# Optimization experiments

Hardware: AMD Instinct MI355X
Metric: run time of the kernel (lower is better)

The kernel has to match this reference:

```python
import jax, jax.numpy as jnp
import numpy as np

N = 100000   # nodes
E = 1600000  # edges (before self-loops)
C = 128      # num_node_features == graph_hidden_channels (residuals require equality)
NHID = 512
NOUT = 256
B = 512      # number of graphs in the batch
BN_EPS = 1e-5


def setup_inputs() -> dict:
    key = jax.random.key(0)
    ks = list(jax.random.split(key, 32))
    k = iter(ks)

    def w(shape, fan_in):
        return jax.random.normal(next(k), shape, jnp.float32) * (1.0 / np.sqrt(fan_in))

    inp = {}
    inp["x"] = jax.random.normal(next(k), (N, C), jnp.float32)
    inp["edge_index"] = jax.random.randint(next(k), (2, E), 0, N, jnp.int32)
    inp["batch"] = jnp.sort(jax.random.randint(next(k), (N,), 0, B, jnp.int32))
    # three GCN layers: lin weight [C,C], bias [C], BN gamma/beta
    for i in (1, 2, 3):
        inp[f"W{i}"] = w((C, C), C)
        inp[f"b{i}"] = jnp.zeros((C,), jnp.float32)
        inp[f"g{i}"] = jnp.ones((C,), jnp.float32)
        inp[f"be{i}"] = jnp.zeros((C,), jnp.float32)
    # GAT (1 head)
    inp["Wa"] = w((C, C), C)
    inp["asrc"] = w((C,), C)
    inp["adst"] = w((C,), C)
    inp["ba"] = jnp.zeros((C,), jnp.float32)
    inp["ga"] = jnp.ones((C,), jnp.float32)
    inp["bea"] = jnp.zeros((C,), jnp.float32)
    # MLP head
    inp["Wh1"] = w((C, NHID), C)
    inp["bh1"] = jnp.zeros((NHID,), jnp.float32)
    inp["Wm0"] = w((NHID, NHID), NHID)
    inp["bm0"] = jnp.zeros((NHID,), jnp.float32)
    inp["Wm1"] = w((NHID, NHID), NHID)
    inp["bm1"] = jnp.zeros((NHID,), jnp.float32)
    inp["Wo"] = w((NHID, NOUT), NHID)
    inp["bo"] = jnp.zeros((NOUT,), jnp.float32)
    return inp


def _add_self_loops(edge_index):
    loops = jnp.arange(N, dtype=edge_index.dtype)
    src = jnp.concatenate([edge_index[0], loops])
    dst = jnp.concatenate([edge_index[1], loops])
    return src, dst


def _gcn(x, src, dst, W, b):
    # PyG GCNConv: add self-loops, D^-1/2 (A+I) D^-1/2 (x W) + b
    deg = jax.ops.segment_sum(jnp.ones_like(dst, jnp.float32), dst, num_segments=N)
    dinv = jax.lax.rsqrt(jnp.maximum(deg, 1.0))
    norm = dinv[src] * dinv[dst]                      # [E+N]
    h = x @ W                                         # [N,C]
    msg = h[src] * norm[:, None]                      # gather + scale
    return jax.ops.segment_sum(msg, dst, num_segments=N) + b


def _gat(x, src, dst, W, asrc, adst, b):
    # PyG GATConv, heads=1: self-loops, alpha = softmax_dst(leaky_relu(a_s.h_j + a_d.h_i))
    h = x @ W                                         # [N,C]
    es = (h * asrc).sum(-1)                           # [N]
    ed = (h * adst).sum(-1)
    e = jax.nn.leaky_relu(es[src] + ed[dst], 0.2)     # [E+N]
    m = jax.ops.segment_max(e, dst, num_segments=N)
    ex = jnp.exp(e - m[dst])
    s = jax.ops.segment_sum(ex, dst, num_segments=N)
    alpha = ex / (s[dst] + 1e-16)
    out = jax.ops.segment_sum(h[src] * alpha[:, None], dst, num_segments=N)
    return out + b


def _bn(h, g, be):
    # BatchNorm in training mode: biased batch stats over node dim
    m = h.mean(0)
    v = ((h - m) ** 2).mean(0)
    return (h - m) * jax.lax.rsqrt(v + BN_EPS) * g + be


def reference(x, edge_index, batch,
              W1, b1, g1, be1, W2, b2, g2, be2, W3, b3, g3, be3,
              Wa, asrc, adst, ba, ga, bea,
              Wh1, bh1, Wm0, bm0, Wm1, bm1, Wo, bo):
    src, dst = _add_self_loops(edge_index)
    x = jax.nn.relu(_bn(_gcn(x, src, dst, W1, b1), g1, be1)) + x
    x = jax.nn.relu(_bn(_gcn(x, src, dst, W2, b2), g2, be2)) + x
    x = jax.nn.relu(_bn(_gcn(x, src, dst, W3, b3), g3, be3)) + x
    x = jax.nn.relu(_bn(_gat(x, src, dst, Wa, asrc, adst, ba), ga, bea)) + x
    # global mean pool over graphs
    sums = jax.ops.segment_sum(x, batch, num_segments=B)
    cnt = jax.ops.segment_sum(jnp.ones((N,), jnp.float32), batch, num_segments=B)
    x = sums / jnp.maximum(cnt, 1.0)[:, None]         # [B,C]
    x = jax.nn.relu(x @ Wh1 + bh1)
    x = jax.nn.relu(x @ Wm0 + bm0)
    x = jax.nn.relu(x @ Wm1 + bm1)
    return x @ Wo + bo                                # [B,NOUT]
```

## Files before the change

kernel.cpp:

```cpp
#include <hip/hip_runtime.h>

#define N_NODES 100000
#define N_EDGES 1600000
#define CCH     128
#define BG      512
#define NHID    512
#define NOUT    256
#define BN_EPS  1e-5f

typedef __attribute__((ext_vector_type(8))) short s16x8;
typedef __attribute__((ext_vector_type(4))) float f32x4;

static __device__ __forceinline__ float leaky(float x) { return x > 0.f ? x : 0.2f * x; }
static __device__ __forceinline__ uint32_t bfr16(float x) {
  uint32_t u = __float_as_uint(x);
  u += 0x7fffu + ((u >> 16) & 1u);
  return u >> 16;
}
static __device__ __forceinline__ uint32_t pack2(float a, float b) {
  return bfr16(a) | (bfr16(b) << 16);
}
static __device__ __forceinline__ float blo(uint32_t u) { return __uint_as_float(u << 16); }
static __device__ __forceinline__ float bhi(uint32_t u) { return __uint_as_float(u & 0xffff0000u); }

__global__ void hist_kernel(const int* __restrict__ dst, int* __restrict__ indeg) {
  int e = blockIdx.x * 256 + threadIdx.x;
  if (e < N_EDGES) atomicAdd(&indeg[dst[e]], 1);
}

__global__ __launch_bounds__(256) void scan_chunks(const int* __restrict__ indeg,
                                                   int* __restrict__ rowstart,
                                                   int* __restrict__ chunksum) {
  int tid = threadIdx.x;
  int base = blockIdx.x * 1024 + tid * 4;
  int4 v;
  if (base + 3 < N_NODES) {
    v = *(const int4*)(indeg + base);
  } else {
    v.x = (base + 0 < N_NODES) ? indeg[base + 0] : 0;
    v.y = (base + 1 < N_NODES) ? indeg[base + 1] : 0;
    v.z = (base + 2 < N_NODES) ? indeg[base + 2] : 0;
    v.w = (base + 3 < N_NODES) ? indeg[base + 3] : 0;
  }
  int s = v.x + v.y + v.z + v.w;
  __shared__ int ss[256];
  ss[tid] = s;
  __syncthreads();
  for (int off = 1; off < 256; off <<= 1) {
    int t = (tid >= off) ? ss[tid - off] : 0;
    __syncthreads();
    ss[tid] += t;
    __syncthreads();
  }
  int excl = ss[tid] - s;
  if (base + 0 < N_NODES) rowstart[base + 0] = excl;
  if (base + 1 < N_NODES) rowstart[base + 1] = excl + v.x;
  if (base + 2 < N_NODES) rowstart[base + 2] = excl + v.x + v.y;
  if (base + 3 < N_NODES) rowstart[base + 3] = excl + v.x + v.y + v.z;
  if (tid == 255) chunksum[blockIdx.x] = ss[255];
}

__global__ void scan_sums(int* __restrict__ chunksum, int nch) {
  __shared__ int ss[128];
  int tid = threadIdx.x;
  int v = (tid < nch) ? chunksum[tid] : 0;
  ss[tid] = v;
  __syncthreads();
  for (int off = 1; off < 128; off <<= 1) {
    int t = (tid >= off) ? ss[tid - off] : 0;
    __syncthreads();
    ss[tid] += t;
    __syncthreads();
  }
  if (tid < nch) chunksum[tid] = ss[tid] - v;
}

__global__ void scan_add(int* __restrict__ rowstart, const int* __restrict__ chunksum) {
  int i = blockIdx.x * 256 + threadIdx.x;
  if (i < N_NODES)      rowstart[i] += chunksum[i >> 10];
  else if (i == N_NODES) rowstart[N_NODES] = N_EDGES;
}

__global__ void compute_dinv(const int* __restrict__ indeg, float* __restrict__ dinv) {
  int i = blockIdx.x * 256 + threadIdx.x;
  if (i < N_NODES) dinv[i] = rsqrtf((float)(indeg[i] + 1));
}

__global__ void scatter_edges(const int* __restrict__ src, const int* __restrict__ dst,
                              const int* __restrict__ rowstart, int* __restrict__ cursor,
                              const float* __restrict__ dinv, int2* __restrict__ csr_sw) {
  int e = blockIdx.x * 256 + threadIdx.x;
  if (e < N_EDGES) {
    int d = dst[e];
    int s = src[e];
    int p = rowstart[d] + atomicAdd(&cursor[d], 1);
    float w = dinv[s] * dinv[d];
    csr_sw[p] = make_int2(s, __float_as_int(w));
  }
}

__global__ void cast_bf16_kernel(const float2* __restrict__ x2, uint32_t* __restrict__ xb) {
  size_t idx = (size_t)blockIdx.x * 256 + threadIdx.x;
  if (idx >= (size_t)N_NODES * 64) return;
  float2 v = x2[idx];
  xb[idx] = pack2(v.x, v.y);
}

__global__ void pack_w_kernel(const float* __restrict__ W, unsigned short* __restrict__ Wp) {
  int t = blockIdx.x * 256 + threadIdx.x;
  if (t >= 2048) return;
  int lane = t & 63;
  int ks = (t >> 6) & 3;
  int nt = t >> 8;
  int c = nt * 16 + (lane & 15);
  int kb = ks * 32 + (lane >> 4) * 8;
#pragma unroll
  for (int i = 0; i < 8; ++i)
    Wp[(size_t)t * 8 + i] = (unsigned short)bfr16(W[(size_t)(kb + i) * 128 + c]);
}

__global__ __launch_bounds__(256) void gemm_mfma(const uint32_t* __restrict__ Ab,
                                                 const unsigned short* __restrict__ Wp,
                                                 uint32_t* __restrict__ Hb,
                                                 int M) {
  int wave = threadIdx.x >> 6, lane = threadIdx.x & 63;
  int row0 = blockIdx.x * 128 + wave * 32;
  const unsigned short* A16 = (const unsigned short*)Ab;

  f32x4 acc[2][8];
#pragma unroll
  for (int mt = 0; mt < 2; ++mt)
#pragma unroll
    for (int nt = 0; nt < 8; ++nt) acc[mt][nt] = (f32x4){0.f, 0.f, 0.f, 0.f};

  s16x8 a[2][4];
  int r = lane & 15, ko = (lane >> 4) * 8;
#pragma unroll
  for (int mt = 0; mt < 2; ++mt) {
    int row = row0 + mt * 16 + r;
    bool v = row < M;
    const unsigned short* ap = A16 + (size_t)row * 128 + ko;
#pragma unroll
    for (int ks = 0; ks < 4; ++ks) {
      s16x8 af = {0, 0, 0, 0, 0, 0, 0, 0};
      if (v) af = *(const s16x8*)(ap + ks * 32);
      a[mt][ks] = af;
    }
  }
#pragma unroll
  for (int ks = 0; ks < 4; ++ks) {
#pragma unroll
    for (int nt = 0; nt < 8; ++nt) {
      s16x8 b = *(const s16x8*)(Wp + ((size_t)(nt * 4 + ks) * 64 + lane) * 8);
      acc[0][nt] = __builtin_amdgcn_mfma_f32_16x16x32_bf16(a[0][ks], b, acc[0][nt], 0, 0, 0);
      acc[1][nt] = __builtin_amdgcn_mfma_f32_16x16x32_bf16(a[1][ks], b, acc[1][nt], 0, 0, 0);
    }
  }
#pragma unroll
  for (int mt = 0; mt < 2; ++mt) {
#pragma unroll
    for (int nt = 0; nt < 8; ++nt) {
#pragma unroll
      for (int reg = 0; reg < 4; ++reg) {
        float v0 = acc[mt][nt][reg];
        float v1 = __shfl_xor(v0, 1);
        int row = row0 + mt * 16 + (lane >> 4) * 4 + reg;
        int col = nt * 16 + (lane & 15);
        if (!(lane & 1) && row < M)
          Hb[(size_t)row * 64 + (col >> 1)] = pack2(v0, v1);
      }
    }
  }
}

__global__ __launch_bounds__(256) void gcn_agg(const uint2* __restrict__ Hb2,
                                               const int* __restrict__ rowstart,
                                               const int2* __restrict__ csr_sw,
                                               const float* __restrict__ dinv,
                                               float4* __restrict__ agg4,
                                               float* __restrict__ stats) {
  int tid = threadIdx.x;
  int lane = tid & 63;
  int hl = lane & 31;
  int half = lane >> 5;
  int gw = (blockIdx.x * 256 + tid) >> 6;
  int nw = (gridDim.x * 256) >> 6;
  float s0 = 0, s1 = 0, s2 = 0, s3 = 0, q0 = 0, q1 = 0, q2 = 0, q3 = 0;
  for (int pi = gw; pi < N_NODES / 2; pi += nw) {
    int n = 2 * pi + half;
    int e0 = rowstart[n], e1 = rowstart[n + 1];
    int len = e1 - e0;
    int G = (len + 3) >> 2;
    int Gmax = max(G, __shfl_xor(G, 32));
    int ecl = (len > 0) ? (e1 - 1) : 0;
    float di = dinv[n];
    uint2 hs = Hb2[(size_t)n * 32 + hl];
    float ws = di * di;
    float c0 = blo(hs.x) * ws, c1 = bhi(hs.x) * ws;
    float c2 = blo(hs.y) * ws, c3 = bhi(hs.y) * ws;
    int sI0, sI1, sI2, sI3;
    float w0, w1, w2, w3;
    {
      int e = e0;
      int2 pa = csr_sw[e < e1 ? e : ecl];
      int2 pb = csr_sw[e + 1 < e1 ? e + 1 : ecl];
      int2 pc = csr_sw[e + 2 < e1 ? e + 2 : ecl];
      int2 pd = csr_sw[e + 3 < e1 ? e + 3 : ecl];
      sI0 = pa.x; w0 = (e < e1) ? __int_as_float(pa.y) : 0.f;
      sI1 = pb.x; w1 = (e + 1 < e1) ? __int_as_float(pb.y) : 0.f;
      sI2 = pc.x; w2 = (e + 2 < e1) ? __int_as_float(pc.y) : 0.f;
      sI3 = pd.x; w3 = (e + 3 < e1) ? __int_as_float(pd.y) : 0.f;
    }
    for (int g = 0; g < Gmax; ++g) {
      uint2 r0 = Hb2[(size_t)sI0 * 32 + hl];
      uint2 r1 = Hb2[(size_t)sI1 * 32 + hl];
      uint2 r2 = Hb2[(size_t)sI2 * 32 + hl];
      uint2 r3 = Hb2[(size_t)sI3 * 32 + hl];
      float cw0 = w0, cw1 = w1, cw2 = w2, cw3 = w3;
      int e = e0 + (g + 1) * 4;
      int2 pa = csr_sw[e < e1 ? e : ecl];
      int2 pb = csr_sw[e + 1 < e1 ? e + 1 : ecl];
      int2 pc = csr_sw[e + 2 < e1 ? e + 2 : ecl];
      int2 pd = csr_sw[e + 3 < e1 ? e + 3 : ecl];
      sI0 = pa.x; w0 = (e < e1) ? __int_as_float(pa.y) : 0.f;
      sI1 = pb.x; w1 = (e + 1 < e1) ? __int_as_float(pb.y) : 0.f;
      sI2 = pc.x; w2 = (e + 2 < e1) ? __int_as_float(pc.y) : 0.f;
      sI3 = pd.x; w3 = (e + 3 < e1) ? __int_as_float(pd.y) : 0.f;
      c0 = fmaf(blo(r0.x), cw0, c0); c1 = fmaf(bhi(r0.x), cw0, c1);
      c2 = fmaf(blo(r0.y), cw0, c2); c3 = fmaf(bhi(r0.y), cw0, c3);
      c0 = fmaf(blo(r1.x), cw1, c0); c1 = fmaf(bhi(r1.x), cw1, c1);
      c2 = fmaf(blo(r1.y), cw1, c2); c3 = fmaf(bhi(r1.y), cw1, c3);
      c0 = fmaf(blo(r2.x), cw2, c0); c1 = fmaf(bhi(r2.x), cw2, c1);
      c2 = fmaf(blo(r2.y), cw2, c2); c3 = fmaf(bhi(r2.y), cw2, c3);
      c0 = fmaf(blo(r3.x), cw3, c0); c1 = fmaf(bhi(r3.x), cw3, c1);
      c2 = fmaf(blo(r3.y), cw3, c2); c3 = fmaf(bhi(r3.y), cw3, c3);
    }
    agg4[(size_t)n * 32 + hl] = make_float4(c0, c1, c2, c3);
    s0 += c0; s1 += c1; s2 += c2; s3 += c3;
    q0 += c0 * c0; q1 += c1 * c1; q2 += c2 * c2; q3 += c3 * c3;
  }
  s0 += __shfl_xor(s0, 32); s1 += __shfl_xor(s1, 32);
  s2 += __shfl_xor(s2, 32); s3 += __shfl_xor(s3, 32);
  q0 += __shfl_xor(q0, 32); q1 += __shfl_xor(q1, 32);
  q2 += __shfl_xor(q2, 32); q3 += __shfl_xor(q3, 32);
  __shared__ float red[4][128];
  int w = tid >> 6;
  if (half == 0) {
    red[w][4 * hl + 0] = s0; red[w][4 * hl + 1] = s1;
    red[w][4 * hl + 2] = s2; red[w][4 * hl + 3] = s3;
  }
  __syncthreads();
  if (w == 0) {
    float a = red[0][2 * lane] + red[1][2 * lane] + red[2][2 * lane] + red[3][2 * lane];
    float b = red[0][2 * lane + 1] + red[1][2 * lane + 1] + red[2][2 * lane + 1] + red[3][2 * lane + 1];
    atomicAdd(&stats[2 * lane], a);
    atomicAdd(&stats[2 * lane + 1], b);
  }
  __syncthreads();
  if (half == 0) {
    red[w][4 * hl + 0] = q0; red[w][4 * hl + 1] = q1;
    red[w][4 * hl + 2] = q2; red[w][4 * hl + 3] = q3;
  }
  __syncthreads();
  if (w == 0) {
    float a = red[0][2 * lane] + red[1][2 * lane] + red[2][2 * lane] + red[3][2 * lane];
    float b = red[0][2 * lane + 1] + red[1][2 * lane + 1] + red[2][2 * lane + 1] + red[3][2 * lane + 1];
    atomicAdd(&stats[128 + 2 * lane], a);
    atomicAdd(&stats[128 + 2 * lane + 1], b);
  }
}

__global__ __launch_bounds__(256) void compute_esed(const uint32_t* __restrict__ Hb,
                                                    const float* __restrict__ asrc,
                                                    const float* __restrict__ adst,
                                                    float* __restrict__ es, float* __restrict__ ed) {
  int lane = threadIdx.x & 63;
  int gwave = (blockIdx.x * 256 + threadIdx.x) >> 6;
  if (gwave >= N_NODES) return;
  float2 av = ((const float2*)asrc)[lane];
  float2 dv = ((const float2*)adst)[lane];
  uint32_t hv = Hb[(size_t)gwave * 64 + lane];
  float hx = blo(hv), hy = bhi(hv);
  float e_s = hx * av.x + hy * av.y;
  float e_d = hx * dv.x + hy * dv.y;
  for (int off = 32; off; off >>= 1) {
    e_s += __shfl_down(e_s, off);
    e_d += __shfl_down(e_d, off);
  }
  if (lane == 0) { es[gwave] = e_s; ed[gwave] = e_d; }
}

__global__ void gat_pack_kernel(int2* __restrict__ sw, const float* __restrict__ es) {
  int e = blockIdx.x * 256 + threadIdx.x;
  if (e < N_EDGES) {
    int2 v = sw[e];
    v.y = __float_as_int(es[v.x]);
    sw[e] = v;
  }
}

__global__ __launch_bounds__(256) void gat_agg(const uint2* __restrict__ Hb2,
                                               const int* __restrict__ rowstart,
                                               const int2* __restrict__ gpack,
                                               const float* __restrict__ es,
                                               const float* __restrict__ ed,
                                               float4* __restrict__ agg4,
                                               float* __restrict__ stats) {
  int tid = threadIdx.x;
  int lane = tid & 63;
  int hl = lane & 31;
  int half = lane >> 5;
  int gw = (blockIdx.x * 256 + tid) >> 6;
  int nw = (gridDim.x * 256) >> 6;
  float s0 = 0, s1 = 0, s2 = 0, s3 = 0, q0 = 0, q1 = 0, q2 = 0, q3 = 0;
  for (int pi = gw; pi < N_NODES / 2; pi += nw) {
    int n = 2 * pi + half;
    int e0 = rowstart[n], e1 = rowstart[n + 1];
    int len = e1 - e0;
    int G = (len + 3) >> 2;
    int Gmax = max(G, __shfl_xor(G, 32));
    int ecl = (len > 0) ? (e1 - 1) : 0;
    float edi = ed[n], esi = es[n];
    float wself = __expf(leaky(esi + edi));
    float wsum = (hl == 0) ? wself : 0.f;
    for (int e = e0 + hl; e < e1; e += 32)
      wsum += __expf(leaky(__int_as_float(gpack[e].y) + edi));
#pragma unroll
    for (int off = 16; off; off >>= 1) wsum += __shfl_xor(wsum, off);
    float inv = 1.f / (wsum + 1e-16f);

    uint2 hs = Hb2[(size_t)n * 32 + hl];
    float wS = wself * inv;
    float c0 = blo(hs.x) * wS, c1 = bhi(hs.x) * wS;
    float c2 = blo(hs.y) * wS, c3 = bhi(hs.y) * wS;
    int sI0, sI1, sI2, sI3;
    float w0, w1, w2, w3;
    {
      int e = e0;
      int2 pa = gpack[e < e1 ? e : ecl];
      int2 pb = gpack[e + 1 < e1 ? e + 1 : ecl];
      int2 pc = gpack[e + 2 < e1 ? e + 2 : ecl];
      int2 pd = gpack[e + 3 < e1 ? e + 3 : ecl];
      sI0 = pa.x; w0 = (e < e1) ? __expf(leaky(__int_as_float(pa.y) + edi)) * inv : 0.f;
      sI1 = pb.x; w1 = (e + 1 < e1) ? __expf(leaky(__int_as_float(pb.y) + edi)) * inv : 0.f;
      sI2 = pc.x; w2 = (e + 2 < e1) ? __expf(leaky(__int_as_float(pc.y) + edi)) * inv : 0.f;
      sI3 = pd.x; w3 = (e + 3 < e1) ? __expf(leaky(__int_as_float(pd.y) + edi)) * inv : 0.f;
    }
    for (int g = 0; g < Gmax; ++g) {
      uint2 r0 = Hb2[(size_t)sI0 * 32 + hl];
      uint2 r1 = Hb2[(size_t)sI1 * 32 + hl];
      uint2 r2 = Hb2[(size_t)sI2 * 32 + hl];
      uint2 r3 = Hb2[(size_t)sI3 * 32 + hl];
      float cw0 = w0, cw1 = w1, cw2 = w2, cw3 = w3;
      int e = e0 + (g + 1) * 4;
      int2 pa = gpack[e < e1 ? e : ecl];
      int2 pb = gpack[e + 1 < e1 ? e + 1 : ecl];
      int2 pc = gpack[e + 2 < e1 ? e + 2 : ecl];
      int2 pd = gpack[e + 3 < e1 ? e + 3 : ecl];
      sI0 = pa.x; w0 = (e < e1) ? __expf(leaky(__int_as_float(pa.y) + edi)) * inv : 0.f;
      sI1 = pb.x; w1 = (e + 1 < e1) ? __expf(leaky(__int_as_float(pb.y) + edi)) * inv : 0.f;
      sI2 = pc.x; w2 = (e + 2 < e1) ? __expf(leaky(__int_as_float(pc.y) + edi)) * inv : 0.f;
      sI3 = pd.x; w3 = (e + 3 < e1) ? __expf(leaky(__int_as_float(pd.y) + edi)) * inv : 0.f;
      c0 = fmaf(blo(r0.x), cw0, c0); c1 = fmaf(bhi(r0.x), cw0, c1);
      c2 = fmaf(blo(r0.y), cw0, c2); c3 = fmaf(bhi(r0.y), cw0, c3);
      c0 = fmaf(blo(r1.x), cw1, c0); c1 = fmaf(bhi(r1.x), cw1, c1);
      c2 = fmaf(blo(r1.y), cw1, c2); c3 = fmaf(bhi(r1.y), cw1, c3);
      c0 = fmaf(blo(r2.x), cw2, c0); c1 = fmaf(bhi(r2.x), cw2, c1);
      c2 = fmaf(blo(r2.y), cw2, c2); c3 = fmaf(bhi(r2.y), cw2, c3);
      c0 = fmaf(blo(r3.x), cw3, c0); c1 = fmaf(bhi(r3.x), cw3, c1);
      c2 = fmaf(blo(r3.y), cw3, c2); c3 = fmaf(bhi(r3.y), cw3, c3);
    }
    agg4[(size_t)n * 32 + hl] = make_float4(c0, c1, c2, c3);
    s0 += c0; s1 += c1; s2 += c2; s3 += c3;
    q0 += c0 * c0; q1 += c1 * c1; q2 += c2 * c2; q3 += c3 * c3;
  }
  s0 += __shfl_xor(s0, 32); s1 += __shfl_xor(s1, 32);
  s2 += __shfl_xor(s2, 32); s3 += __shfl_xor(s3, 32);
  q0 += __shfl_xor(q0, 32); q1 += __shfl_xor(q1, 32);
  q2 += __shfl_xor(q2, 32); q3 += __shfl_xor(q3, 32);
  __shared__ float red[4][128];
  int w = tid >> 6;
  if (half == 0) {
    red[w][4 * hl + 0] = s0; red[w][4 * hl + 1] = s1;
    red[w][4 * hl + 2] = s2; red[w][4 * hl + 3] = s3;
  }
  __syncthreads();
  if (w == 0) {
    float a = red[0][2 * lane] + red[1][2 * lane] + red[2][2 * lane] + red[3][2 * lane];
    float b = red[0][2 * lane + 1] + red[1][2 * lane + 1] + red[2][2 * lane + 1] + red[3][2 * lane + 1];
    atomicAdd(&stats[2 * lane], a);
    atomicAdd(&stats[2 * lane + 1], b);
  }
  __syncthreads();
  if (half == 0) {
    red[w][4 * hl + 0] = q0; red[w][4 * hl + 1] = q1;
    red[w][4 * hl + 2] = q2; red[w][4 * hl + 3] = q3;
  }
  __syncthreads();
  if (w == 0) {
    float a = red[0][2 * lane] + red[1][2 * lane] + red[2][2 * lane] + red[3][2 * lane];
    float b = red[0][2 * lane + 1] + red[1][2 * lane + 1] + red[2][2 * lane + 1] + red[3][2 * lane + 1];
    atomicAdd(&stats[128 + 2 * lane], a);
    atomicAdd(&stats[128 + 2 * lane + 1], b);
  }
}

__global__ void bn_relu_res(const float4* __restrict__ agg4, const float* __restrict__ stats,
                            const float* __restrict__ gamma, const float* __restrict__ beta,
                            uint2* __restrict__ xb) {
  size_t idx = (size_t)blockIdx.x * 256 + threadIdx.x;
  if (idx >= (size_t)N_NODES * 32) return;
  int c = ((int)(idx & 31)) * 4;
  const float n_inv = 1.f / (float)N_NODES;
  float sc[4], bc[4];
#pragma unroll
  for (int k = 0; k < 4; ++k) {
    float m = stats[c + k] * n_inv;
    float v = stats[128 + c + k] * n_inv - m * m;
    sc[k] = gamma[c + k] * rsqrtf(v + BN_EPS);
    bc[k] = beta[c + k] - m * sc[k];
  }
  float4 a = agg4[idx];
  uint2 xi = xb[idx];
  float r0 = fmaxf(fmaf(a.x, sc[0], bc[0]), 0.f) + blo(xi.x);
  float r1 = fmaxf(fmaf(a.y, sc[1], bc[1]), 0.f) + bhi(xi.x);
  float r2 = fmaxf(fmaf(a.z, sc[2], bc[2]), 0.f) + blo(xi.y);
  float r3 = fmaxf(fmaf(a.w, sc[3], bc[3]), 0.f) + bhi(xi.y);
  xb[idx] = make_uint2(pack2(r0, r1), pack2(r2, r3));
}

__global__ void graph_starts(const int* __restrict__ batch, int* __restrict__ gstart) {
  int n = blockIdx.x * 256 + threadIdx.x;
  if (n >= N_NODES) return;
  int b = batch[n];
  int bp = (n == 0) ? -1 : batch[n - 1];
  for (int g = bp + 1; g <= b; ++g) gstart[g] = n;
  if (n == N_NODES - 1) {
    for (int g = b + 1; g <= BG; ++g) gstart[g] = N_NODES;
  }
}

__global__ __launch_bounds__(256) void pool_kernel(const uint32_t* __restrict__ xb,
                                                   const int* __restrict__ gstart,
                                                   float* __restrict__ pooled) {
  int g = blockIdx.x;
  int c = threadIdx.x & 127;
  int half = threadIdx.x >> 7;
  int s = gstart[g], e = gstart[g + 1];
  float acc = 0.f;
  for (int n = s + half; n < e; n += 2) {
    uint32_t u = xb[(size_t)n * 64 + (c >> 1)];
    acc += (c & 1) ? bhi(u) : blo(u);
  }
  __shared__ float red[256];
  red[threadIdx.x] = acc;
  __syncthreads();
  if (half == 0) {
    float v = red[c] + red[128 + c];
    int cnt = e - s;
    pooled[(size_t)g * 128 + c] = v / fmaxf((float)cnt, 1.f);
  }
}

template <int RELU, int BIAS>
__global__ __launch_bounds__(256) void gemm_f32(const float* __restrict__ A,
                                                const float* __restrict__ W,
                                                const float* __restrict__ bias,
                                                float* __restrict__ Cmat,
                                                int M, int K, int N) {
  __shared__ float As[32][128];
  __shared__ float Bs[32][128];
  int tid = threadIdx.x;
  int row0 = blockIdx.x * 128, col0 = blockIdx.y * 128;
  int tx = tid & 15, ty = tid >> 4;
  float acc[8][8];
#pragma unroll
  for (int i = 0; i < 8; ++i)
#pragma unroll
    for (int j = 0; j < 8; ++j) acc[i][j] = 0.f;

  for (int k0 = 0; k0 < K; k0 += 32) {
    {
      int r = tid >> 1;
      int kseg = (tid & 1) * 16;
      bool valid = (row0 + r) < M;
      const float* ap = A + (size_t)(row0 + r) * K + k0 + kseg;
#pragma unroll
      for (int q = 0; q < 4; ++q) {
        float4 v;
        if (valid) v = *(const float4*)(ap + q * 4);
        else { v.x = v.y = v.z = v.w = 0.f; }
        As[kseg + q * 4 + 0][r] = v.x;
        As[kseg + q * 4 + 1][r] = v.y;
        As[kseg + q * 4 + 2][r] = v.z;
        As[kseg + q * 4 + 3][r] = v.w;
      }
    }
    {
      int kk = tid >> 3;
      int seg = (tid & 7) * 16;
      const float* wp = W + (size_t)(k0 + kk) * N + col0 + seg;
#pragma unroll
      for (int q = 0; q < 4; ++q)
        *(float4*)&Bs[kk][seg + q * 4] = *(const float4*)(wp + q * 4);
    }
    __syncthreads();
#pragma unroll
    for (int kk = 0; kk < 32; ++kk) {
      float4 a0 = *(const float4*)&As[kk][ty * 4];
      float4 a1 = *(const float4*)&As[kk][64 + ty * 4];
      float4 b0 = *(const float4*)&Bs[kk][tx * 4];
      float4 b1 = *(const float4*)&Bs[kk][64 + tx * 4];
      float av[8] = {a0.x, a0.y, a0.z, a0.w, a1.x, a1.y, a1.z, a1.w};
      float bv[8] = {b0.x, b0.y, b0.z, b0.w, b1.x, b1.y, b1.z, b1.w};
#pragma unroll
      for (int i = 0; i < 8; ++i)
#pragma unroll
        for (int j = 0; j < 8; ++j) acc[i][j] = fmaf(av[i], bv[j], acc[i][j]);
    }
    __syncthreads();
  }
#pragma unroll
  for (int i = 0; i < 8; ++i) {
    int r = row0 + ((i < 4) ? (ty * 4 + i) : (64 + ty * 4 + i - 4));
    if (r >= M) continue;
#pragma unroll
    for (int j = 0; j < 8; ++j) {
      int c = col0 + ((j < 4) ? (tx * 4 + j) : (64 + tx * 4 + j - 4));
      float v = acc[i][j];
      if (BIAS) v += bias[c];
      if (RELU) v = fmaxf(v, 0.f);
      Cmat[(size_t)r * N + c] = v;
    }
  }
}

extern "C" void kernel_launch(void* const* d_in, const int* in_sizes, int n_in,
                              void* d_out, int out_size, void* d_ws, size_t ws_size,
                              hipStream_t stream) {
  const float* x_in  = (const float*)d_in[0];
  const int*   eidx  = (const int*)d_in[1];
  const int*   batch = (const int*)d_in[2];
  const float* W1 = (const float*)d_in[3];
  const float* g1 = (const float*)d_in[5];
  const float* be1 = (const float*)d_in[6];
  const float* W2 = (const float*)d_in[7];
  const float* g2 = (const float*)d_in[9];
  const float* be2 = (const float*)d_in[10];
  const float* W3 = (const float*)d_in[11];
  const float* g3 = (const float*)d_in[13];
  const float* be3 = (const float*)d_in[14];
  const float* Wa = (const float*)d_in[15];
  const float* asrc = (const float*)d_in[16];
  const float* adst = (const float*)d_in[17];
  const float* ga = (const float*)d_in[19];
  const float* bea = (const float*)d_in[20];
  const float* Wh1 = (const float*)d_in[21];
  const float* bh1 = (const float*)d_in[22];
  const float* Wm0 = (const float*)d_in[23];
  const float* bm0 = (const float*)d_in[24];
  const float* Wm1 = (const float*)d_in[25];
  const float* bm1 = (const float*)d_in[26];
  const float* Wo = (const float*)d_in[27];
  const float* bo = (const float*)d_in[28];

  const int* src = eidx;
  const int* dst = eidx + N_EDGES;

  char* p = (char*)d_ws;
  auto alloc = [&](size_t bytes) {
    char* r = p;
    p += (bytes + 255) & ~(size_t)255;
    return r;
  };
  uint32_t* Hb     = (uint32_t*)alloc((size_t)N_NODES * 64 * 4);
  uint32_t* xb     = (uint32_t*)alloc((size_t)N_NODES * 64 * 4);
  float* agg       = (float*)alloc((size_t)N_NODES * CCH * 4);
  int2*  csr_sw    = (int2*)alloc((size_t)N_EDGES * 8);
  int*   rowstart  = (int*)alloc((size_t)(N_NODES + 1) * 4);
  int*   indeg     = (int*)alloc((size_t)2 * N_NODES * 4);
  int*   cursor    = indeg + N_NODES;
  float* dinv      = (float*)alloc((size_t)N_NODES * 4);
  float* es        = (float*)alloc((size_t)N_NODES * 4);
  float* ed        = (float*)alloc((size_t)N_NODES * 4);
  int*   chunksum  = (int*)alloc(128 * 4);
  float* stats     = (float*)alloc(4 * 256 * 4);
  int*   gstart    = (int*)alloc((BG + 1) * 4);
  float* pooled    = (float*)alloc((size_t)BG * CCH * 4);
  float* m1        = (float*)alloc((size_t)BG * NHID * 4);
  float* m2        = (float*)alloc((size_t)BG * NHID * 4);
  unsigned short* Wp1 = (unsigned short*)alloc(2048 * 8 * 2);
  unsigned short* Wp2 = (unsigned short*)alloc(2048 * 8 * 2);
  unsigned short* Wp3 = (unsigned short*)alloc(2048 * 8 * 2);
  unsigned short* Wp4 = (unsigned short*)alloc(2048 * 8 * 2);

  hipMemsetAsync(indeg, 0, (size_t)2 * N_NODES * 4, stream);
  hipMemsetAsync(stats, 0, 4 * 256 * 4, stream);

  hist_kernel<<<(N_EDGES + 255) / 256, 256, 0, stream>>>(dst, indeg);
  scan_chunks<<<98, 256, 0, stream>>>(indeg, rowstart, chunksum);
  scan_sums<<<1, 128, 0, stream>>>(chunksum, 98);
  scan_add<<<(N_NODES + 256) / 256, 256, 0, stream>>>(rowstart, chunksum);
  compute_dinv<<<(N_NODES + 255) / 256, 256, 0, stream>>>(indeg, dinv);
  scatter_edges<<<(N_EDGES + 255) / 256, 256, 0, stream>>>(src, dst, rowstart, cursor, dinv, csr_sw);

  const int el2_blocks = (N_NODES * 64 + 255) / 256;
  const int el4_blocks = (N_NODES * 32 + 255) / 256;
  cast_bf16_kernel<<<el2_blocks, 256, 0, stream>>>((const float2*)x_in, xb);
  pack_w_kernel<<<8, 256, 0, stream>>>(W1, Wp1);
  pack_w_kernel<<<8, 256, 0, stream>>>(W2, Wp2);
  pack_w_kernel<<<8, 256, 0, stream>>>(W3, Wp3);
  pack_w_kernel<<<8, 256, 0, stream>>>(Wa, Wp4);

  const int gemm_blocks_m = (N_NODES + 127) / 128;
  const int AGG_BLOCKS = 2048;

  const unsigned short* Wps[3] = {Wp1, Wp2, Wp3};
  const float* gs[3] = {g1, g2, g3};
  const float* bes[3] = {be1, be2, be3};
  for (int l = 0; l < 3; ++l) {
    gemm_mfma<<<gemm_blocks_m, 256, 0, stream>>>(xb, Wps[l], Hb, N_NODES);
    gcn_agg<<<AGG_BLOCKS, 256, 0, stream>>>((const uint2*)Hb, rowstart, csr_sw, dinv,
                                            (float4*)agg, stats + l * 256);
    bn_relu_res<<<el4_blocks, 256, 0, stream>>>((const float4*)agg, stats + l * 256,
                                                gs[l], bes[l], (uint2*)xb);
  }

  gemm_mfma<<<gemm_blocks_m, 256, 0, stream>>>(xb, Wp4, Hb, N_NODES);
  compute_esed<<<(N_NODES + 3) / 4, 256, 0, stream>>>(Hb, asrc, adst, es, ed);
  gat_pack_kernel<<<(N_EDGES + 255) / 256, 256, 0, stream>>>(csr_sw, es);
  gat_agg<<<AGG_BLOCKS, 256, 0, stream>>>((const uint2*)Hb, rowstart, csr_sw, es, ed,
                                          (float4*)agg, stats + 3 * 256);
  bn_relu_res<<<el4_blocks, 256, 0, stream>>>((const float4*)agg, stats + 3 * 256,
                                              ga, bea, (uint2*)xb);

  graph_starts<<<(N_NODES + 255) / 256, 256, 0, stream>>>(batch, gstart);
  pool_kernel<<<BG, 256, 0, stream>>>(xb, gstart, pooled);

  gemm_f32<1, 1><<<dim3(4, 4), 256, 0, stream>>>(pooled, Wh1, bh1, m1, BG, CCH, NHID);
  gemm_f32<1, 1><<<dim3(4, 4), 256, 0, stream>>>(m1, Wm0, bm0, m2, BG, NHID, NHID);
  gemm_f32<1, 1><<<dim3(4, 4), 256, 0, stream>>>(m2, Wm1, bm1, m1, BG, NHID, NHID);
  gemm_f32<0, 1><<<dim3(4, 2), 256, 0, stream>>>(m1, Wo, bo, (float*)d_out, BG, NHID, NOUT);
}
```

Before: 1.182 ms.

## Deepen gather prefetch in aggregation and precompute GAT edge weights per node

```diff
diff --git a/kernel.cpp b/kernel.cpp
--- a/kernel.cpp
+++ b/kernel.cpp
@@ -173,12 +173,15 @@
   }
 }
 
-__global__ __launch_bounds__(256) void gcn_agg(const uint2* __restrict__ Hb2,
-                                               const int* __restrict__ rowstart,
-                                               const int2* __restrict__ csr_sw,
-                                               const float* __restrict__ dinv,
-                                               float4* __restrict__ agg4,
-                                               float* __restrict__ stats) {
+template <int GAT>
+__global__ __launch_bounds__(256) void agg_kernel(const uint2* __restrict__ Hb2,
+                                                  const int* __restrict__ rowstart,
+                                                  const int2* __restrict__ pack,
+                                                  const float* __restrict__ dinv,
+                                                  const float* __restrict__ wselfa,
+                                                  const float* __restrict__ winv,
+                                                  float4* __restrict__ agg4,
+                                                  float* __restrict__ stats) {
   int tid = threadIdx.x;
   int lane = tid & 63;
   int hl = lane & 31;
@@ -193,48 +196,81 @@
     int G = (len + 3) >> 2;
     int Gmax = max(G, __shfl_xor(G, 32));
     int ecl = (len > 0) ? (e1 - 1) : 0;
-    float di = dinv[n];
+    float selfw, fscale;
+    if (GAT) { selfw = wselfa[n]; fscale = winv[n]; }
+    else     { float di = dinv[n]; selfw = di * di; fscale = 1.f; }
     uint2 hs = Hb2[(size_t)n * 32 + hl];
-    float ws = di * di;
-    float c0 = blo(hs.x) * ws, c1 = bhi(hs.x) * ws;
-    float c2 = blo(hs.y) * ws, c3 = bhi(hs.y) * ws;
-    int sI0, sI1, sI2, sI3;
-    float w0, w1, w2, w3;
-    {
-      int e = e0;
-      int2 pa = csr_sw[e < e1 ? e : ecl];
-      int2 pb = csr_sw[e + 1 < e1 ? e + 1 : ecl];
-      int2 pc = csr_sw[e + 2 < e1 ? e + 2 : ecl];
-      int2 pd = csr_sw[e + 3 < e1 ? e + 3 : ecl];
-      sI0 = pa.x; w0 = (e < e1) ? __int_as_float(pa.y) : 0.f;
-      sI1 = pb.x; w1 = (e + 1 < e1) ? __int_as_float(pb.y) : 0.f;
-      sI2 = pc.x; w2 = (e + 2 < e1) ? __int_as_float(pc.y) : 0.f;
-      sI3 = pd.x; w3 = (e + 3 < e1) ? __int_as_float(pd.y) : 0.f;
-    }
-    for (int g = 0; g < Gmax; ++g) {
-      uint2 r0 = Hb2[(size_t)sI0 * 32 + hl];
-      uint2 r1 = Hb2[(size_t)sI1 * 32 + hl];
-      uint2 r2 = Hb2[(size_t)sI2 * 32 + hl];
-      uint2 r3 = Hb2[(size_t)sI3 * 32 + hl];
-      float cw0 = w0, cw1 = w1, cw2 = w2, cw3 = w3;
-      int e = e0 + (g + 1) * 4;
-      int2 pa = csr_sw[e < e1 ? e : ecl];
-      int2 pb = csr_sw[e + 1 < e1 ? e + 1 : ecl];
-      int2 pc = csr_sw[e + 2 < e1 ? e + 2 : ecl];
-      int2 pd = csr_sw[e + 3 < e1 ? e + 3 : ecl];
-      sI0 = pa.x; w0 = (e < e1) ? __int_as_float(pa.y) : 0.f;
-      sI1 = pb.x; w1 = (e + 1 < e1) ? __int_as_float(pb.y) : 0.f;
-      sI2 = pc.x; w2 = (e + 2 < e1) ? __int_as_float(pc.y) : 0.f;
-      sI3 = pd.x; w3 = (e + 3 < e1) ? __int_as_float(pd.y) : 0.f;
-      c0 = fmaf(blo(r0.x), cw0, c0); c1 = fmaf(bhi(r0.x), cw0, c1);
-      c2 = fmaf(blo(r0.y), cw0, c2); c3 = fmaf(bhi(r0.y), cw0, c3);
-      c0 = fmaf(blo(r1.x), cw1, c0); c1 = fmaf(bhi(r1.x), cw1, c1);
-      c2 = fmaf(blo(r1.y), cw1, c2); c3 = fmaf(bhi(r1.y), cw1, c3);
-      c0 = fmaf(blo(r2.x), cw2, c0); c1 = fmaf(bhi(r2.x), cw2, c1);
-      c2 = fmaf(blo(r2.y), cw2, c2); c3 = fmaf(bhi(r2.y), cw2, c3);
-      c0 = fmaf(blo(r3.x), cw3, c0); c1 = fmaf(bhi(r3.x), cw3, c1);
-      c2 = fmaf(blo(r3.y), cw3, c2); c3 = fmaf(bhi(r3.y), cw3, c3);
-    }
+    float c0 = blo(hs.x) * selfw, c1 = bhi(hs.x) * selfw;
+    float c2 = blo(hs.y) * selfw, c3 = bhi(hs.y) * selfw;
+
+    if (Gmax > 0) {
+      uint2 rA0, rA1, rA2, rA3;
+      float wA0, wA1, wA2, wA3;
+      int iB0, iB1, iB2, iB3;
+      float wB0 = 0, wB1 = 0, wB2 = 0, wB3 = 0;
+      iB0 = iB1 = iB2 = iB3 = 0;
+      {
+        int e = e0;
+        int2 pa = pack[e < e1 ? e : ecl];
+        int2 pb = pack[e + 1 < e1 ? e + 1 : ecl];
+        int2 pc = pack[e + 2 < e1 ? e + 2 : ecl];
+        int2 pd = pack[e + 3 < e1 ? e + 3 : ecl];
+        wA0 = (e < e1) ? __int_as_float(pa.y) : 0.f;
+        wA1 = (e + 1 < e1) ? __int_as_float(pb.y) : 0.f;
+        wA2 = (e + 2 < e1) ? __int_as_float(pc.y) : 0.f;
+        wA3 = (e + 3 < e1) ? __int_as_float(pd.y) : 0.f;
+        rA0 = Hb2[(size_t)pa.x * 32 + hl];
+        rA1 = Hb2[(size_t)pb.x * 32 + hl];
+        rA2 = Hb2[(size_t)pc.x * 32 + hl];
+        rA3 = Hb2[(size_t)pd.x * 32 + hl];
+      }
+      if (Gmax > 1) {
+        int e = e0 + 4;
+        int2 pa = pack[e < e1 ? e : ecl];
+        int2 pb = pack[e + 1 < e1 ? e + 1 : ecl];
+        int2 pc = pack[e + 2 < e1 ? e + 2 : ecl];
+        int2 pd = pack[e + 3 < e1 ? e + 3 : ecl];
+        iB0 = pa.x; wB0 = (e < e1) ? __int_as_float(pa.y) : 0.f;
+        iB1 = pb.x; wB1 = (e + 1 < e1) ? __int_as_float(pb.y) : 0.f;
+        iB2 = pc.x; wB2 = (e + 2 < e1) ? __int_as_float(pc.y) : 0.f;
+        iB3 = pd.x; wB3 = (e + 3 < e1) ? __int_as_float(pd.y) : 0.f;
+      }
+      for (int g = 0; g < Gmax; ++g) {
+        uint2 rB0, rB1, rB2, rB3;
+        int nI0, nI1, nI2, nI3;
+        float nw0, nw1, nw2, nw3;
+        if (g + 1 < Gmax) {
+          rB0 = Hb2[(size_t)iB0 * 32 + hl];
+          rB1 = Hb2[(size_t)iB1 * 32 + hl];
+          rB2 = Hb2[(size_t)iB2 * 32 + hl];
+          rB3 = Hb2[(size_t)iB3 * 32 + hl];
+        }
+        if (g + 2 < Gmax) {
+          int e = e0 + (g + 2) * 4;
+          int2 pa = pack[e < e1 ? e : ecl];
+          int2 pb = pack[e + 1 < e1 ? e + 1 : ecl];
+          int2 pc = pack[e + 2 < e1 ? e + 2 : ecl];
+          int2 pd = pack[e + 3 < e1 ? e + 3 : ecl];
+          nI0 = pa.x; nw0 = (e < e1) ? __int_as_float(pa.y) : 0.f;
+          nI1 = pb.x; nw1 = (e + 1 < e1) ? __int_as_float(pb.y) : 0.f;
+          nI2 = pc.x; nw2 = (e + 2 < e1) ? __int_as_float(pc.y) : 0.f;
+          nI3 = pd.x; nw3 = (e + 3 < e1) ? __int_as_float(pd.y) : 0.f;
+        }
+        c0 = fmaf(blo(rA0.x), wA0, c0); c1 = fmaf(bhi(rA0.x), wA0, c1);
+        c2 = fmaf(blo(rA0.y), wA0, c2); c3 = fmaf(bhi(rA0.y), wA0, c3);
+        c0 = fmaf(blo(rA1.x), wA1, c0); c1 = fmaf(bhi(rA1.x), wA1, c1);
+        c2 = fmaf(blo(rA1.y), wA1, c2); c3 = fmaf(bhi(rA1.y), wA1, c3);
+        c0 = fmaf(blo(rA2.x), wA2, c0); c1 = fmaf(bhi(rA2.x), wA2, c1);
+        c2 = fmaf(blo(rA2.y), wA2, c2); c3 = fmaf(bhi(rA2.y), wA2, c3);
+        c0 = fmaf(blo(rA3.x), wA3, c0); c1 = fmaf(bhi(rA3.x), wA3, c1);
+        c2 = fmaf(blo(rA3.y), wA3, c2); c3 = fmaf(bhi(rA3.y), wA3, c3);
+        rA0 = rB0; rA1 = rB1; rA2 = rB2; rA3 = rB3;
+        wA0 = wB0; wA1 = wB1; wA2 = wB2; wA3 = wB3;
+        iB0 = nI0; iB1 = nI1; iB2 = nI2; iB3 = nI3;
+        wB0 = nw0; wB1 = nw1; wB2 = nw2; wB3 = nw3;
+      }
+    }
+    if (GAT) { c0 *= fscale; c1 *= fscale; c2 *= fscale; c3 *= fscale; }
     agg4[(size_t)n * 32 + hl] = make_float4(c0, c1, c2, c3);
     s0 += c0; s1 += c1; s2 += c2; s3 += c3;
     q0 += c0 * c0; q1 += c1 * c1; q2 += c2 * c2; q3 += c3 * c3;
@@ -290,119 +326,23 @@
   if (lane == 0) { es[gwave] = e_s; ed[gwave] = e_d; }
 }
 
-__global__ void gat_pack_kernel(int2* __restrict__ sw, const float* __restrict__ es) {
-  int e = blockIdx.x * 256 + threadIdx.x;
-  if (e < N_EDGES) {
-    int2 v = sw[e];
-    v.y = __float_as_int(es[v.x]);
-    sw[e] = v;
-  }
-}
-
-__global__ __launch_bounds__(256) void gat_agg(const uint2* __restrict__ Hb2,
-                                               const int* __restrict__ rowstart,
-                                               const int2* __restrict__ gpack,
-                                               const float* __restrict__ es,
-                                               const float* __restrict__ ed,
-                                               float4* __restrict__ agg4,
-                                               float* __restrict__ stats) {
-  int tid = threadIdx.x;
-  int lane = tid & 63;
-  int hl = lane & 31;
-  int half = lane >> 5;
-  int gw = (blockIdx.x * 256 + tid) >> 6;
-  int nw = (gridDim.x * 256) >> 6;
-  float s0 = 0, s1 = 0, s2 = 0, s3 = 0, q0 = 0, q1 = 0, q2 = 0, q3 = 0;
-  for (int pi = gw; pi < N_NODES / 2; pi += nw) {
-    int n = 2 * pi + half;
-    int e0 = rowstart[n], e1 = rowstart[n + 1];
-    int len = e1 - e0;
-    int G = (len + 3) >> 2;
-    int Gmax = max(G, __shfl_xor(G, 32));
-    int ecl = (len > 0) ? (e1 - 1) : 0;
-    float edi = ed[n], esi = es[n];
-    float wself = __expf(leaky(esi + edi));
-    float wsum = (hl == 0) ? wself : 0.f;
-    for (int e = e0 + hl; e < e1; e += 32)
-      wsum += __expf(leaky(__int_as_float(gpack[e].y) + edi));
-#pragma unroll
-    for (int off = 16; off; off >>= 1) wsum += __shfl_xor(wsum, off);
-    float inv = 1.f / (wsum + 1e-16f);
-
-    uint2 hs = Hb2[(size_t)n * 32 + hl];
-    float wS = wself * inv;
-    float c0 = blo(hs.x) * wS, c1 = bhi(hs.x) * wS;
-    float c2 = blo(hs.y) * wS, c3 = bhi(hs.y) * wS;
-    int sI0, sI1, sI2, sI3;
-    float w0, w1, w2, w3;
-    {
-      int e = e0;
-      int2 pa = gpack[e < e1 ? e : ecl];
-      int2 pb = gpack[e + 1 < e1 ? e + 1 : ecl];
-      int2 pc = gpack[e + 2 < e1 ? e + 2 : ecl];
-      int2 pd = gpack[e + 3 < e1 ? e + 3 : ecl];
-      sI0 = pa.x; w0 = (e < e1) ? __expf(leaky(__int_as_float(pa.y) + edi)) * inv : 0.f;
-      sI1 = pb.x; w1 = (e + 1 < e1) ? __expf(leaky(__int_as_float(pb.y) + edi)) * inv : 0.f;
-      sI2 = pc.x; w2 = (e + 2 < e1) ? __expf(leaky(__int_as_float(pc.y) + edi)) * inv : 0.f;
-      sI3 = pd.x; w3 = (e + 3 < e1) ? __expf(leaky(__int_as_float(pd.y) + edi)) * inv : 0.f;
-    }
-    for (int g = 0; g < Gmax; ++g) {
-      uint2 r0 = Hb2[(size_t)sI0 * 32 + hl];
-      uint2 r1 = Hb2[(size_t)sI1 * 32 + hl];
-      uint2 r2 = Hb2[(size_t)sI2 * 32 + hl];
-      uint2 r3 = Hb2[(size_t)sI3 * 32 + hl];
-      float cw0 = w0, cw1 = w1, cw2 = w2, cw3 = w3;
-      int e = e0 + (g + 1) * 4;
-      int2 pa = gpack[e < e1 ? e : ecl];
-      int2 pb = gpack[e + 1 < e1 ? e + 1 : ecl];
-      int2 pc = gpack[e + 2 < e1 ? e + 2 : ecl];
-      int2 pd = gpack[e + 3 < e1 ? e + 3 : ecl];
-      sI0 = pa.x; w0 = (e < e1) ? __expf(leaky(__int_as_float(pa.y) + edi)) * inv : 0.f;
-      sI1 = pb.x; w1 = (e + 1 < e1) ? __expf(leaky(__int_as_float(pb.y) + edi)) * inv : 0.f;
-      sI2 = pc.x; w2 = (e + 2 < e1) ? __expf(leaky(__int_as_float(pc.y) + edi)) * inv : 0.f;
-      sI3 = pd.x; w3 = (e + 3 < e1) ? __expf(leaky(__int_as_float(pd.y) + edi)) * inv : 0.f;
-      c0 = fmaf(blo(r0.x), cw0, c0); c1 = fmaf(bhi(r0.x), cw0, c1);
-      c2 = fmaf(blo(r0.y), cw0, c2); c3 = fmaf(bhi(r0.y), cw0, c3);
-      c0 = fmaf(blo(r1.x), cw1, c0); c1 = fmaf(bhi(r1.x), cw1, c1);
-      c2 = fmaf(blo(r1.y), cw1, c2); c3 = fmaf(bhi(r1.y), cw1, c3);
-      c0 = fmaf(blo(r2.x), cw2, c0); c1 = fmaf(bhi(r2.x), cw2, c1);
-      c2 = fmaf(blo(r2.y), cw2, c2); c3 = fmaf(bhi(r2.y), cw2, c3);
-      c0 = fmaf(blo(r3.x), cw3, c0); c1 = fmaf(bhi(r3.x), cw3, c1);
-      c2 = fmaf(blo(r3.y), cw3, c2); c3 = fmaf(bhi(r3.y), cw3, c3);
-    }
-    agg4[(size_t)n * 32 + hl] = make_float4(c0, c1, c2, c3);
-    s0 += c0; s1 += c1; s2 += c2; s3 += c3;
-    q0 += c0 * c0; q1 += c1 * c1; q2 += c2 * c2; q3 += c3 * c3;
-  }
-  s0 += __shfl_xor(s0, 32); s1 += __shfl_xor(s1, 32);
-  s2 += __shfl_xor(s2, 32); s3 += __shfl_xor(s3, 32);
-  q0 += __shfl_xor(q0, 32); q1 += __shfl_xor(q1, 32);
-  q2 += __shfl_xor(q2, 32); q3 += __shfl_xor(q3, 32);
-  __shared__ float red[4][128];
-  int w = tid >> 6;
-  if (half == 0) {
-    red[w][4 * hl + 0] = s0; red[w][4 * hl + 1] = s1;
-    red[w][4 * hl + 2] = s2; red[w][4 * hl + 3] = s3;
-  }
-  __syncthreads();
-  if (w == 0) {
-    float a = red[0][2 * lane] + red[1][2 * lane] + red[2][2 * lane] + red[3][2 * lane];
-    float b = red[0][2 * lane + 1] + red[1][2 * lane + 1] + red[2][2 * lane + 1] + red[3][2 * lane + 1];
-    atomicAdd(&stats[2 * lane], a);
-    atomicAdd(&stats[2 * lane + 1], b);
-  }
-  __syncthreads();
-  if (half == 0) {
-    red[w][4 * hl + 0] = q0; red[w][4 * hl + 1] = q1;
-    red[w][4 * hl + 2] = q2; red[w][4 * hl + 3] = q3;
-  }
-  __syncthreads();
-  if (w == 0) {
-    float a = red[0][2 * lane] + red[1][2 * lane] + red[2][2 * lane] + red[3][2 * lane];
-    float b = red[0][2 * lane + 1] + red[1][2 * lane + 1] + red[2][2 * lane + 1] + red[3][2 * lane + 1];
-    atomicAdd(&stats[128 + 2 * lane], a);
-    atomicAdd(&stats[128 + 2 * lane + 1], b);
-  }
+__global__ void gat_prep_node(int2* __restrict__ pack, const int* __restrict__ rowstart,
+                              const float* __restrict__ es, const float* __restrict__ ed,
+                              float* __restrict__ wselfa, float* __restrict__ winv) {
+  int n = blockIdx.x * 256 + threadIdx.x;
+  if (n >= N_NODES) return;
+  int e0 = rowstart[n], e1 = rowstart[n + 1];
+  float edi = ed[n];
+  float wself = __expf(leaky(es[n] + edi));
+  float s = wself;
+  for (int e = e0; e < e1; ++e) {
+    int sidx = pack[e].x;
+    float w = __expf(leaky(es[sidx] + edi));
+    pack[e].y = __float_as_int(w);
+    s += w;
+  }
+  wselfa[n] = wself;
+  winv[n] = 1.f / (s + 1e-16f);
 }
 
 __global__ void bn_relu_res(const float4* __restrict__ agg4, const float* __restrict__ stats,
@@ -583,6 +523,8 @@
   float* dinv      = (float*)alloc((size_t)N_NODES * 4);
   float* es        = (float*)alloc((size_t)N_NODES * 4);
   float* ed        = (float*)alloc((size_t)N_NODES * 4);
+  float* wselfa    = (float*)alloc((size_t)N_NODES * 4);
+  float* winv      = (float*)alloc((size_t)N_NODES * 4);
   int*   chunksum  = (int*)alloc(128 * 4);
   float* stats     = (float*)alloc(4 * 256 * 4);
   int*   gstart    = (int*)alloc((BG + 1) * 4);
@@ -620,17 +562,17 @@
   const float* bes[3] = {be1, be2, be3};
   for (int l = 0; l < 3; ++l) {
     gemm_mfma<<<gemm_blocks_m, 256, 0, stream>>>(xb, Wps[l], Hb, N_NODES);
-    gcn_agg<<<AGG_BLOCKS, 256, 0, stream>>>((const uint2*)Hb, rowstart, csr_sw, dinv,
-                                            (float4*)agg, stats + l * 256);
+    agg_kernel<0><<<AGG_BLOCKS, 256, 0, stream>>>((const uint2*)Hb, rowstart, csr_sw, dinv,
+                                                  nullptr, nullptr, (float4*)agg, stats + l * 256);
     bn_relu_res<<<el4_blocks, 256, 0, stream>>>((const float4*)agg, stats + l * 256,
                                                 gs[l], bes[l], (uint2*)xb);
   }
 
   gemm_mfma<<<gemm_blocks_m, 256, 0, stream>>>(xb, Wp4, Hb, N_NODES);
   compute_esed<<<(N_NODES + 3) / 4, 256, 0, stream>>>(Hb, asrc, adst, es, ed);
-  gat_pack_kernel<<<(N_EDGES + 255) / 256, 256, 0, stream>>>(csr_sw, es);
-  gat_agg<<<AGG_BLOCKS, 256, 0, stream>>>((const uint2*)Hb, rowstart, csr_sw, es, ed,
-                                          (float4*)agg, stats + 3 * 256);
+  gat_prep_node<<<(N_NODES + 255) / 256, 256, 0, stream>>>(csr_sw, rowstart, es, ed, wselfa, winv);
+  agg_kernel<1><<<AGG_BLOCKS, 256, 0, stream>>>((const uint2*)Hb, rowstart, csr_sw, nullptr,
+                                                wselfa, winv, (float4*)agg, stats + 3 * 256);
   bn_relu_res<<<el4_blocks, 256, 0, stream>>>((const float4*)agg, stats + 3 * 256,
                                               ga, bea, (uint2*)xb);
 
```

After: 1.201 ms. No clear change (+1.6%).
